# Kernel optimization log

Measured on AMD Instinct MI355X. Metric: run time of the kernel, lower is better.

## Reference

```python
import jax, jax.numpy as jnp
import numpy as np

N_NODES = 50000
N_GRAPHS = 512


def _gcn_layer(x, src, dst, W, b):
    # DGL GraphConv, norm='both', allow_zero_in_degree=True
    n = x.shape[0]
    ones = jnp.ones(src.shape[0], x.dtype)
    deg_out = jnp.zeros(n, x.dtype).at[src].add(ones)
    deg_in = jnp.zeros(n, x.dtype).at[dst].add(ones)
    norm_out = jax.lax.rsqrt(jnp.maximum(deg_out, 1.0))
    norm_in = jax.lax.rsqrt(jnp.maximum(deg_in, 1.0))
    h = x * norm_out[:, None]
    agg = jax.ops.segment_sum(h[src], dst, num_segments=n)  # SpMM
    return (agg * norm_in[:, None]) @ W + b


def setup_inputs() -> dict:
    key = jax.random.key(0)
    ks = jax.random.split(key, 16)
    E = 800000
    inp = {
        'nid': jax.random.randint(ks[0], (N_NODES,), 0, 100000),
        'z': jax.random.randint(ks[1], (N_NODES,), 0, 1000),
        'src': jax.random.randint(ks[2], (E,), 0, N_NODES),
        'dst': jax.random.randint(ks[3], (E,), 0, N_NODES),
        'graph_id': jnp.sort(jax.random.randint(ks[4], (N_NODES,), 0, N_GRAPHS)),
        'init_embed': jax.random.normal(ks[5], (100000, 64), jnp.float32) * 0.1,
        'z_table': jax.random.normal(ks[6], (1000, 64), jnp.float32) * 0.1,
        'W0': jax.random.normal(ks[7], (128, 128), jnp.float32) * 0.1,
        'b0': jnp.zeros((128,), jnp.float32),
        'W1': jax.random.normal(ks[8], (128, 128), jnp.float32) * 0.1,
        'b1': jnp.zeros((128,), jnp.float32),
        'W2': jax.random.normal(ks[9], (128, 128), jnp.float32) * 0.1,
        'b2': jnp.zeros((128,), jnp.float32),
        'lin1_W': jax.random.normal(ks[10], (128, 128), jnp.float32) * 0.1,
        'lin1_b': jnp.zeros((128,), jnp.float32),
        'lin2_W': jax.random.normal(ks[11], (128, 200), jnp.float32) * 0.1,
        'lin2_b': jnp.zeros((200,), jnp.float32),
    }
    return inp


def reference(nid, z, src, dst, graph_id, init_embed, z_table, W0, b0, W1, b1, W2, b2, lin1_W, lin1_b, lin2_W, lin2_b):
    # node features: entity embedding lookup + structural label embedding, concat
    x = jnp.concatenate([init_embed[nid], z_table[z]], axis=1)  # [N, 128]
    # layers[:-1] with relu (dropout is identity in eval mode)
    x = jax.nn.relu(_gcn_layer(x, src, dst, W0, b0))
    x = jax.nn.relu(_gcn_layer(x, src, dst, W1, b1))
    x = _gcn_layer(x, src, dst, W2, b2)
    # SumPooling over subgraphs in the batch
    g = jax.ops.segment_sum(x, graph_id, num_segments=N_GRAPHS)  # [G, 128]
    h = jax.nn.relu(g @ lin1_W + lin1_b)
    return h @ lin2_W + lin2_b  # [G, num_rel]
```

## Files before the change

kernel.cpp:

```cpp
#include <hip/hip_runtime.h>
#include <hip/hip_bf16.h>


#define FEAT 128
#define NG 512
#define CH 128
#define NPMAX 12544
#define LDW 136

typedef __attribute__((ext_vector_type(8))) short bf16x8;
typedef __attribute__((ext_vector_type(4))) float f32x4;

__device__ __forceinline__ float bf2f(unsigned short u) {
    union { unsigned int i; float f; } v; v.i = ((unsigned int)u) << 16; return v.f;
}
__device__ __forceinline__ unsigned short f2bf(float f) {
    unsigned int u = __float_as_uint(f);
    return (unsigned short)((u + 0x7FFFu + ((u >> 16) & 1u)) >> 16);
}
__device__ __forceinline__ float lo16(unsigned u) { return __uint_as_float(u << 16); }
__device__ __forceinline__ float hi16(unsigned u) { return __uint_as_float(u & 0xFFFF0000u); }

__global__ __launch_bounds__(256) void k_hist(
        const int* __restrict__ src, const int* __restrict__ dst,
        unsigned* __restrict__ partial_out, unsigned* __restrict__ partial_in,
        int E, int NP, int Ec) {
    __shared__ unsigned h[NPMAX];
    int tid = threadIdx.x;
    int b = blockIdx.x;
    int c = b & (CH - 1);
    const int* __restrict__ arr = (b < CH) ? src : dst;
    unsigned* __restrict__ outp = ((b < CH) ? partial_out : partial_in) + (size_t)c * NP;
    for (int i = tid; i < NP; i += 256) h[i] = 0;
    __syncthreads();
    int e0 = c * Ec, e1 = min(E, e0 + Ec);
    for (int e = e0 + tid; e < e1; e += 256) {
        int v = arr[e];
        atomicAdd(&h[v >> 2], 1u << ((v & 3) * 8));
    }
    __syncthreads();
    for (int i = tid; i < NP; i += 256) outp[i] = h[i];
}

__global__ void k_merge(unsigned* __restrict__ partial_out, unsigned* __restrict__ partial_in,
                        int* __restrict__ cnt_in, float* __restrict__ norm_out,
                        float* __restrict__ norm_in, int N, int NP) {
    int w = blockIdx.x * blockDim.x + threadIdx.x;
    if (w >= NP) return;
    unsigned run_in = 0, run_out = 0;
    for (int c = 0; c < CH; c++) {
        size_t idx = (size_t)c * NP + w;
        unsigned v = partial_in[idx];
        partial_in[idx] = run_in;
        run_in += v;
        run_out += partial_out[idx];
    }
    #pragma unroll
    for (int j = 0; j < 4; j++) {
        int node = w * 4 + j;
        if (node < N) {
            unsigned di = (run_in  >> (j * 8)) & 255u;
            unsigned dd = (run_out >> (j * 8)) & 255u;
            cnt_in[node]   = (int)di;
            norm_in[node]  = rsqrtf(fmaxf((float)di, 1.0f));
            norm_out[node] = rsqrtf(fmaxf((float)dd, 1.0f));
        }
    }
}

__global__ void k_scan_local(const int* __restrict__ cnt, int* __restrict__ excl,
                             int* __restrict__ bsum, int N) {
    __shared__ int s[256];
    int x = threadIdx.x;
    int i = blockIdx.x * 256 + x;
    int v = (i < N) ? cnt[i] : 0;
    s[x] = v;
    __syncthreads();
    for (int off = 1; off < 256; off <<= 1) {
        int t = (x >= off) ? s[x - off] : 0;
        __syncthreads();
        s[x] += t;
        __syncthreads();
    }
    if (i < N) excl[i] = s[x] - v;
    if (x == 255) bsum[blockIdx.x] = s[255];
}

__global__ void k_scan_bsum_prep(int* __restrict__ bsum, int* __restrict__ boff, int nb,
                                 const float* __restrict__ W0, const float* __restrict__ W1,
                                 unsigned short* __restrict__ WF0, unsigned short* __restrict__ WF1) {
    if (blockIdx.x == 0) {
        __shared__ int s[256];
        int x = threadIdx.x;
        int v = (x < nb) ? bsum[x] : 0;
        s[x] = v;
        __syncthreads();
        for (int off = 1; off < 256; off <<= 1) {
            int t = (x >= off) ? s[x - off] : 0;
            __syncthreads();
            s[x] += t;
            __syncthreads();
        }
        if (x < nb) boff[x] = s[x] - v;
    } else {
        int t = ((int)blockIdx.x - 1) * 256 + threadIdx.x;
        const float* __restrict__ W = (t < 16384) ? W0 : W1;
        unsigned short* __restrict__ WF = (t < 16384) ? WF0 : WF1;
        int tt = t & 16383;
        int f = tt >> 9, l = (tt >> 3) & 63, e = tt & 7;
        int n = (f >> 2) * 16 + (l & 15);
        int k = (f & 3) * 32 + (l >> 4) * 8 + e;
        WF[tt] = f2bf(W[k * 128 + n]);
    }
}

__global__ void k_add_off(int* __restrict__ row_start, const int* __restrict__ boff,
                          float* __restrict__ g, int N) {
    int i = blockIdx.x * blockDim.x + threadIdx.x;
    int stride = gridDim.x * blockDim.x;
    if (i < N) row_start[i] += boff[i >> 8];
    for (int j = i; j < NG * FEAT; j += stride) g[j] = 0.f;
}

__global__ __launch_bounds__(256) void k_fill_bx(
        const int* __restrict__ src, const int* __restrict__ dst,
        const int* __restrict__ row_start, const unsigned* __restrict__ partial_in,
        unsigned short* __restrict__ csr,
        const int* __restrict__ nid, const int* __restrict__ z,
        const float* __restrict__ emb, const float* __restrict__ zt,
        const float* __restrict__ nout, unsigned short* __restrict__ x,
        int N, int E, int NP, int Ec) {
    if ((int)blockIdx.x < CH) {
        __shared__ unsigned cur[NPMAX];
        int tid = threadIdx.x;
        int c = blockIdx.x;
        const unsigned* __restrict__ pre = partial_in + (size_t)c * NP;
        for (int i = tid; i < NP; i += 256) cur[i] = pre[i];
        __syncthreads();
        int e0 = c * Ec, e1 = min(E, e0 + Ec);
        for (int e = e0 + tid; e < e1; e += 256) {
            int d = dst[e], s = src[e];
            int sh = (d & 3) * 8;
            unsigned t = atomicAdd(&cur[d >> 2], 1u << sh);
            int off = (int)((t >> sh) & 255u);
            csr[row_start[d] + off] = (unsigned short)s;
        }
    } else {
        int tid = ((int)blockIdx.x - CH) * 256 + threadIdx.x;
        int i = tid >> 5, q = tid & 31;
        if (i < N) {
            float4 v;
            if (q < 16) v = ((const float4*)emb)[(size_t)nid[i] * 16 + q];
            else        v = ((const float4*)zt)[(size_t)z[i] * 16 + (q - 16)];
            float w = nout[i];
            ushort4 u;
            u.x = f2bf(v.x * w); u.y = f2bf(v.y * w);
            u.z = f2bf(v.z * w); u.w = f2bf(v.w * w);
            ((ushort4*)x)[(size_t)i * 32 + q] = u;
        }
    }
}

#define ACC8(u)                                                                  \
    a0 += lo16(u.x); a1 += hi16(u.x); a2 += lo16(u.y); a3 += hi16(u.y);          \
    a4 += lo16(u.z); a5 += hi16(u.z); a6 += lo16(u.w); a7 += hi16(u.w);

#define GATHER_LOOP                                                              \
    {                                                                            \
        int base = row_start[node];                                              \
        int n = cnt_in[node];                                                    \
        const uint4* xp = (const uint4*)x;                   \
        for (int j0 = 0; j0 < n; j0 += 16) {                                     \
            int rem = n - j0;                                                    \
            int m = rem < 16 ? rem : 16;                                         \
            int e = (int)csr[base + j0 + (ql < m ? ql : 0)];                     \
            int j = 0;                                                           \
            for (; j + 8 <= m; j += 8) {                                         \
                int s0 = __shfl(e, j + 0, 16), s1 = __shfl(e, j + 1, 16);        \
                int s2 = __shfl(e, j + 2, 16), s3 = __shfl(e, j + 3, 16);        \
                int s4 = __shfl(e, j + 4, 16), s5 = __shfl(e, j + 5, 16);        \
                int s6 = __shfl(e, j + 6, 16), s7 = __shfl(e, j + 7, 16);        \
                uint4 u0 = xp[(size_t)s0 * 16 + ql];                             \
                uint4 u1 = xp[(size_t)s1 * 16 + ql];                             \
                uint4 u2 = xp[(size_t)s2 * 16 + ql];                             \
                uint4 u3 = xp[(size_t)s3 * 16 + ql];                             \
                uint4 u4 = xp[(size_t)s4 * 16 + ql];                             \
                uint4 u5 = xp[(size_t)s5 * 16 + ql];                             \
                uint4 u6 = xp[(size_t)s6 * 16 + ql];                             \
                uint4 u7 = xp[(size_t)s7 * 16 + ql];                             \
                ACC8(u0) ACC8(u1) ACC8(u2) ACC8(u3)                              \
                ACC8(u4) ACC8(u5) ACC8(u6) ACC8(u7)                              \
            }                                                                    \
            for (; j + 4 <= m; j += 4) {                                         \
                int s0 = __shfl(e, j + 0, 16), s1 = __shfl(e, j + 1, 16);        \
                int s2 = __shfl(e, j + 2, 16), s3 = __shfl(e, j + 3, 16);        \
                uint4 u0 = xp[(size_t)s0 * 16 + ql];                             \
                uint4 u1 = xp[(size_t)s1 * 16 + ql];                             \
                uint4 u2 = xp[(size_t)s2 * 16 + ql];                             \
                uint4 u3 = xp[(size_t)s3 * 16 + ql];                             \
                ACC8(u0) ACC8(u1) ACC8(u2) ACC8(u3)                              \
            }                                                                    \
            for (; j < m; j++) {                                                 \
                int s = __shfl(e, j, 16);                                        \
                uint4 u = xp[(size_t)s * 16 + ql];                               \
                ACC8(u)                                                          \
            }                                                                    \
        }                                                                        \
    }

__global__ __launch_bounds__(256) void k_gather_gemm(
        const unsigned short* __restrict__ x, const float* __restrict__ nin,
        const unsigned short* __restrict__ csr, const int* __restrict__ row_start,
        const int* __restrict__ cnt_in, const unsigned short* __restrict__ WF,
        const float* __restrict__ bias, const float* __restrict__ nout,
        unsigned short* __restrict__ y, int N) {
    __shared__ unsigned short As[64 * LDW];
    int tid = threadIdx.x;
    int nb = blockIdx.x * 64;
    int ql = tid & 15;
    int nsub = tid >> 4;

    #pragma unroll 1
    for (int r = 0; r < 4; r++) {
        int node = nb + r * 16 + nsub;
        float a0 = 0.f, a1 = 0.f, a2 = 0.f, a3 = 0.f;
        float a4 = 0.f, a5 = 0.f, a6 = 0.f, a7 = 0.f;
        if (node < N) {
            GATHER_LOOP
            float ni = nin[node];
            a0 *= ni; a1 *= ni; a2 *= ni; a3 *= ni;
            a4 *= ni; a5 *= ni; a6 *= ni; a7 *= ni;
        }
        uint4 o;
        o.x = (unsigned)f2bf(a0) | ((unsigned)f2bf(a1) << 16);
        o.y = (unsigned)f2bf(a2) | ((unsigned)f2bf(a3) << 16);
        o.z = (unsigned)f2bf(a4) | ((unsigned)f2bf(a5) << 16);
        o.w = (unsigned)f2bf(a6) | ((unsigned)f2bf(a7) << 16);
        *(uint4*)(As + (r * 16 + nsub) * LDW + ql * 8) = o;
    }
    __syncthreads();

    int lane = tid & 63;
    int m0 = (tid >> 6) * 16;
    int c = lane & 15, q = lane >> 4;

    const unsigned short* ap = As + (m0 + c) * LDW + q * 8;
    bf16x8 fa0 = *(const bf16x8*)(ap);
    bf16x8 fa1 = *(const bf16x8*)(ap + 32);
    bf16x8 fa2 = *(const bf16x8*)(ap + 64);
    bf16x8 fa3 = *(const bf16x8*)(ap + 96);
    const bf16x8* __restrict__ wf = (const bf16x8*)WF;

    #pragma unroll
    for (int nt = 0; nt < 8; nt++) {
        bf16x8 fb0 = wf[(nt * 4 + 0) * 64 + lane];
        bf16x8 fb1 = wf[(nt * 4 + 1) * 64 + lane];
        bf16x8 fb2 = wf[(nt * 4 + 2) * 64 + lane];
        bf16x8 fb3 = wf[(nt * 4 + 3) * 64 + lane];
        float bb = bias[nt * 16 + c];
        f32x4 acc = {bb, bb, bb, bb};
        acc = __builtin_amdgcn_mfma_f32_16x16x32_bf16(fa0, fb0, acc, 0, 0, 0);
        acc = __builtin_amdgcn_mfma_f32_16x16x32_bf16(fa1, fb1, acc, 0, 0, 0);
        acc = __builtin_amdgcn_mfma_f32_16x16x32_bf16(fa2, fb2, acc, 0, 0, 0);
        acc = __builtin_amdgcn_mfma_f32_16x16x32_bf16(fa3, fb3, acc, 0, 0, 0);
        #pragma unroll
        for (int rr = 0; rr < 4; rr++) {
            int row = m0 + q * 4 + rr;
            float s = nout[min(nb + row, N - 1)];
            As[row * LDW + nt * 16 + c] = f2bf(fmaxf(acc[rr], 0.f) * s);
        }
    }
    __syncthreads();

    for (int i = tid; i < 64 * 16; i += 256) {
        int row = i >> 4, seg = i & 15;
        int node = nb + row;
        if (node < N) {
            const ushort4* p = (const ushort4*)(As + row * LDW + seg * 8);
            ushort4* d = (ushort4*)(y + (size_t)node * 128 + seg * 8);
            d[0] = p[0]; d[1] = p[1];
        }
    }
}

__global__ __launch_bounds__(256) void k_gather_pool(
        const unsigned short* __restrict__ x, const float* __restrict__ nin,
        const unsigned short* __restrict__ csr, const int* __restrict__ row_start,
        const int* __restrict__ cnt_in, const int* __restrict__ gid,
        float* __restrict__ g, int N) {
    __shared__ float gl[16][FEAT];
    __shared__ int used;
    int tid = threadIdx.x;
    int nb = blockIdx.x * 16;
    for (int i = tid; i < 16 * FEAT; i += 256) ((float*)gl)[i] = 0.f;
    if (tid == 0) used = 0;
    __syncthreads();

    int ql = tid & 15;
    int node = nb + (tid >> 4);
    int g0 = gid[nb];
    float a0 = 0.f, a1 = 0.f, a2 = 0.f, a3 = 0.f;
    float a4 = 0.f, a5 = 0.f, a6 = 0.f, a7 = 0.f;
    int slot = -1;
    if (node < N) {
        GATHER_LOOP
        float ni = nin[node];
        a0 *= ni; a1 *= ni; a2 *= ni; a3 *= ni;
        a4 *= ni; a5 *= ni; a6 *= ni; a7 *= ni;
        slot = gid[node] - g0;
    }
    if (slot >= 16) {
        float* p = g + (size_t)(g0 + slot) * FEAT + ql * 8;
        atomicAdd(p + 0, a0); atomicAdd(p + 1, a1);
        atomicAdd(p + 2, a2); atomicAdd(p + 3, a3);
        atomicAdd(p + 4, a4); atomicAdd(p + 5, a5);
        atomicAdd(p + 6, a6); atomicAdd(p + 7, a7);
    } else if (slot >= 0) {
        float* p = &gl[slot][ql * 8];
        atomicAdd(p + 0, a0); atomicAdd(p + 1, a1);
        atomicAdd(p + 2, a2); atomicAdd(p + 3, a3);
        atomicAdd(p + 4, a4); atomicAdd(p + 5, a5);
        atomicAdd(p + 6, a6); atomicAdd(p + 7, a7);
        if (ql == 0) atomicOr(&used, 1 << slot);
    }
    __syncthreads();
    int u = used;
    #pragma unroll
    for (int s0 = 0; s0 < 16; s0 += 2) {
        int s = s0 + (tid >> 7);
        if ((u >> s) & 1) {
            int j = tid & 127;
            atomicAdd(&g[(size_t)(g0 + s) * FEAT + j], gl[s][j]);
        }
    }
}

__global__ __launch_bounds__(256) void k_head(
        const float* __restrict__ g, const int* __restrict__ gid,
        const float* __restrict__ W2, const float* __restrict__ b2,
        const float* __restrict__ l1W, const float* __restrict__ l1b,
        const float* __restrict__ l2W, const float* __restrict__ l2b,
        float* __restrict__ out, int N) {
    __shared__ float gs[128];
    __shared__ float ys[128];
    __shared__ float hs[128];
    int gi = blockIdx.x, tid = threadIdx.x;

    int lo = 0, hi = N;
    while (lo < hi) { int m = (lo + hi) >> 1; if (gid[m] < gi) lo = m + 1; else hi = m; }
    int s0 = lo;
    lo = 0; hi = N;
    while (lo < hi) { int m = (lo + hi) >> 1; if (gid[m] < gi + 1) lo = m + 1; else hi = m; }
    float cnt = (float)(lo - s0);

    if (tid < 128) gs[tid] = g[(size_t)gi * FEAT + tid];
    __syncthreads();
    if (tid < 128) {
        float a = cnt * b2[tid];
        for (int k = 0; k < 128; k++) a += gs[k] * W2[(size_t)k * 128 + tid];
        ys[tid] = a;
    }
    __syncthreads();
    if (tid < 128) {
        float a = l1b[tid];
        for (int k = 0; k < 128; k++) a += ys[k] * l1W[(size_t)k * 128 + tid];
        hs[tid] = fmaxf(a, 0.f);
    }
    __syncthreads();
    if (tid < 200) {
        float a = l2b[tid];
        for (int k = 0; k < 128; k++) a += hs[k] * l2W[(size_t)k * 200 + tid];
        out[(size_t)gi * 200 + tid] = a;
    }
}

extern "C" void kernel_launch(void* const* d_in, const int* in_sizes, int n_in,
                              void* d_out, int out_size, void* d_ws, size_t ws_size,
                              hipStream_t stream) {
    const int*   nid = (const int*)d_in[0];
    const int*   z   = (const int*)d_in[1];
    const int*   src = (const int*)d_in[2];
    const int*   dst = (const int*)d_in[3];
    const int*   gid = (const int*)d_in[4];
    const float* emb = (const float*)d_in[5];
    const float* zt  = (const float*)d_in[6];
    const float* W0  = (const float*)d_in[7];
    const float* b0  = (const float*)d_in[8];
    const float* W1  = (const float*)d_in[9];
    const float* b1  = (const float*)d_in[10];
    const float* W2  = (const float*)d_in[11];
    const float* b2  = (const float*)d_in[12];
    const float* l1W = (const float*)d_in[13];
    const float* l1b = (const float*)d_in[14];
    const float* l2W = (const float*)d_in[15];
    const float* l2b = (const float*)d_in[16];
    float* out = (float*)d_out;

    const int N = in_sizes[0];
    const int E = in_sizes[2];
    const int NB = (N + 255) / 256;
    const int NP = (N + 3) / 4;
    const int Ec = (E + CH - 1) / CH;

    size_t NA = (size_t)((N + 63) & ~63);
    float* norm_out = (float*)d_ws;
    float* norm_in  = norm_out + NA;
    float* g        = norm_in + NA;
    unsigned short* xA  = (unsigned short*)(g + (size_t)NG * FEAT);
    unsigned short* xB  = xA + (size_t)N * FEAT;
    unsigned short* WF0 = xB + (size_t)N * FEAT;
    unsigned short* WF1 = WF0 + 128 * 128;
    int* cnt_in    = (int*)(WF1 + 128 * 128);
    int* row_start = cnt_in + NA;
    int* bsum      = row_start + NA;
    int* boff      = bsum + 256;
    unsigned* partial_out = (unsigned*)(boff + 256);
    unsigned* partial_in  = partial_out + (size_t)CH * NP;
    unsigned short* csr = (unsigned short*)(partial_in + (size_t)CH * NP);

    k_hist<<<2 * CH, 256, 0, stream>>>(src, dst, partial_out, partial_in, E, NP, Ec);
    k_merge<<<(NP + 255) / 256, 256, 0, stream>>>(partial_out, partial_in, cnt_in,
                                                  norm_out, norm_in, N, NP);
    k_scan_local<<<NB, 256, 0, stream>>>(cnt_in, row_start, bsum, N);
    k_scan_bsum_prep<<<1 + 128, 256, 0, stream>>>(bsum, boff, NB, W0, W1, WF0, WF1);
    k_add_off<<<NB, 256, 0, stream>>>(row_start, boff, g, N);
    int XB = (N * 32 + 255) / 256;
    k_fill_bx<<<CH + XB, 256, 0, stream>>>(src, dst, row_start, partial_in, csr,
                                           nid, z, emb, zt, norm_out, xA, N, E, NP, Ec);

    int gg_blocks = (N + 63) / 64;
    int gp_blocks = (N + 15) / 16;

    k_gather_gemm<<<gg_blocks, 256, 0, stream>>>(xA, norm_in, csr, row_start, cnt_in,
                                                 WF0, b0, norm_out, xB, N);
    k_gather_gemm<<<gg_blocks, 256, 0, stream>>>(xB, norm_in, csr, row_start, cnt_in,
                                                 WF1, b1, norm_out, xA, N);
    k_gather_pool<<<gp_blocks, 256, 0, stream>>>(xA, norm_in, csr, row_start, cnt_in,
                                                 gid, g, N);

    k_head<<<NG, 256, 0, stream>>>(g, gid, W2, b2, l1W, l1b, l2W, l2b, out, N);
}
```

Before: 313.0 us.

## Shrink gather-GEMM tiles to 16 nodes and segment-reduce pooling in shared memory

The gather-GEMM kernel now handles 16 nodes per block instead of 64. Each of the four waves computes two of the eight 16-column output tiles over the same 16 rows, so there are four times as many blocks and no serial four-pass gather loop. This should raise parallelism and latency hiding in the memory-bound gather, at the cost of reloading the weight fragments per block. The pooling kernel replaces per-element LDS atomics and the used-mask with a plain store to shared memory, then a run-length segmented sum over sorted graph ids, issuing one global atomic per run.

Result: faster. 277.8 us (-11.2%).

```diff
diff --git a/kernel.cpp b/kernel.cpp
--- a/kernel.cpp
+++ b/kernel.cpp
@@ -214,45 +214,44 @@
         const int* __restrict__ cnt_in, const unsigned short* __restrict__ WF,
         const float* __restrict__ bias, const float* __restrict__ nout,
         unsigned short* __restrict__ y, int N) {
-    __shared__ unsigned short As[64 * LDW];
+    __shared__ unsigned short As[16 * LDW];
     int tid = threadIdx.x;
-    int nb = blockIdx.x * 64;
+    int nb = blockIdx.x * 16;
     int ql = tid & 15;
-    int nsub = tid >> 4;
-
-    #pragma unroll 1
-    for (int r = 0; r < 4; r++) {
-        int node = nb + r * 16 + nsub;
-        float a0 = 0.f, a1 = 0.f, a2 = 0.f, a3 = 0.f;
-        float a4 = 0.f, a5 = 0.f, a6 = 0.f, a7 = 0.f;
-        if (node < N) {
-            GATHER_LOOP
-            float ni = nin[node];
-            a0 *= ni; a1 *= ni; a2 *= ni; a3 *= ni;
-            a4 *= ni; a5 *= ni; a6 *= ni; a7 *= ni;
-        }
-        uint4 o;
-        o.x = (unsigned)f2bf(a0) | ((unsigned)f2bf(a1) << 16);
-        o.y = (unsigned)f2bf(a2) | ((unsigned)f2bf(a3) << 16);
-        o.z = (unsigned)f2bf(a4) | ((unsigned)f2bf(a5) << 16);
-        o.w = (unsigned)f2bf(a6) | ((unsigned)f2bf(a7) << 16);
-        *(uint4*)(As + (r * 16 + nsub) * LDW + ql * 8) = o;
-    }
+    int nl = tid >> 4;
+    int node = nb + nl;
+
+    float a0 = 0.f, a1 = 0.f, a2 = 0.f, a3 = 0.f;
+    float a4 = 0.f, a5 = 0.f, a6 = 0.f, a7 = 0.f;
+    if (node < N) {
+        GATHER_LOOP
+        float ni = nin[node];
+        a0 *= ni; a1 *= ni; a2 *= ni; a3 *= ni;
+        a4 *= ni; a5 *= ni; a6 *= ni; a7 *= ni;
+    }
+    uint4 o;
+    o.x = (unsigned)f2bf(a0) | ((unsigned)f2bf(a1) << 16);
+    o.y = (unsigned)f2bf(a2) | ((unsigned)f2bf(a3) << 16);
+    o.z = (unsigned)f2bf(a4) | ((unsigned)f2bf(a5) << 16);
+    o.w = (unsigned)f2bf(a6) | ((unsigned)f2bf(a7) << 16);
+    *(uint4*)(As + nl * LDW + ql * 8) = o;
     __syncthreads();
 
     int lane = tid & 63;
-    int m0 = (tid >> 6) * 16;
+    int wv = tid >> 6;
     int c = lane & 15, q = lane >> 4;
 
-    const unsigned short* ap = As + (m0 + c) * LDW + q * 8;
+    const unsigned short* ap = As + c * LDW + q * 8;
     bf16x8 fa0 = *(const bf16x8*)(ap);
     bf16x8 fa1 = *(const bf16x8*)(ap + 32);
     bf16x8 fa2 = *(const bf16x8*)(ap + 64);
     bf16x8 fa3 = *(const bf16x8*)(ap + 96);
     const bf16x8* __restrict__ wf = (const bf16x8*)WF;
+    __syncthreads();
 
     #pragma unroll
-    for (int nt = 0; nt < 8; nt++) {
+    for (int t = 0; t < 2; t++) {
+        int nt = wv * 2 + t;
         bf16x8 fb0 = wf[(nt * 4 + 0) * 64 + lane];
         bf16x8 fb1 = wf[(nt * 4 + 1) * 64 + lane];
         bf16x8 fb2 = wf[(nt * 4 + 2) * 64 + lane];
@@ -265,19 +264,19 @@
         acc = __builtin_amdgcn_mfma_f32_16x16x32_bf16(fa3, fb3, acc, 0, 0, 0);
         #pragma unroll
         for (int rr = 0; rr < 4; rr++) {
-            int row = m0 + q * 4 + rr;
+            int row = q * 4 + rr;
             float s = nout[min(nb + row, N - 1)];
             As[row * LDW + nt * 16 + c] = f2bf(fmaxf(acc[rr], 0.f) * s);
         }
     }
     __syncthreads();
 
-    for (int i = tid; i < 64 * 16; i += 256) {
-        int row = i >> 4, seg = i & 15;
-        int node = nb + row;
-        if (node < N) {
+    {
+        int row = tid >> 4, seg = tid & 15;
+        int nd = nb + row;
+        if (nd < N) {
             const ushort4* p = (const ushort4*)(As + row * LDW + seg * 8);
-            ushort4* d = (ushort4*)(y + (size_t)node * 128 + seg * 8);
+            ushort4* d = (ushort4*)(y + (size_t)nd * 128 + seg * 8);
             d[0] = p[0]; d[1] = p[1];
         }
     }
@@ -288,17 +287,14 @@
         const unsigned short* __restrict__ csr, const int* __restrict__ row_start,
         const int* __restrict__ cnt_in, const int* __restrict__ gid,
         float* __restrict__ g, int N) {
-    __shared__ float gl[16][FEAT];
-    __shared__ int used;
+    __shared__ __align__(16) float gl[16][132];
+    __shared__ int slots[16];
     int tid = threadIdx.x;
     int nb = blockIdx.x * 16;
-    for (int i = tid; i < 16 * FEAT; i += 256) ((float*)gl)[i] = 0.f;
-    if (tid == 0) used = 0;
-    __syncthreads();
-
     int ql = tid & 15;
-    int node = nb + (tid >> 4);
-    int g0 = gid[nb];
+    int nl = tid >> 4;
+    int node = nb + nl;
+
     float a0 = 0.f, a1 = 0.f, a2 = 0.f, a3 = 0.f;
     float a4 = 0.f, a5 = 0.f, a6 = 0.f, a7 = 0.f;
     int slot = -1;
@@ -307,32 +303,29 @@
         float ni = nin[node];
         a0 *= ni; a1 *= ni; a2 *= ni; a3 *= ni;
         a4 *= ni; a5 *= ni; a6 *= ni; a7 *= ni;
-        slot = gid[node] - g0;
-    }
-    if (slot >= 16) {
-        float* p = g + (size_t)(g0 + slot) * FEAT + ql * 8;
-        atomicAdd(p + 0, a0); atomicAdd(p + 1, a1);
-        atomicAdd(p + 2, a2); atomicAdd(p + 3, a3);
-        atomicAdd(p + 4, a4); atomicAdd(p + 5, a5);
-        atomicAdd(p + 6, a6); atomicAdd(p + 7, a7);
-    } else if (slot >= 0) {
-        float* p = &gl[slot][ql * 8];
-        atomicAdd(p + 0, a0); atomicAdd(p + 1, a1);
-        atomicAdd(p + 2, a2); atomicAdd(p + 3, a3);
-        atomicAdd(p + 4, a4); atomicAdd(p + 5, a5);
-        atomicAdd(p + 6, a6); atomicAdd(p + 7, a7);
-        if (ql == 0) atomicOr(&used, 1 << slot);
-    }
-    __syncthreads();
-    int u = used;
+        slot = gid[node];
+    }
+    float4* row = (float4*)&gl[nl][ql * 8];
+    row[0] = make_float4(a0, a1, a2, a3);
+    row[1] = make_float4(a4, a5, a6, a7);
+    if (ql == 0) slots[nl] = slot;
+    __syncthreads();
+
+    int h = tid >> 7;
+    int j = tid & 127;
+    int prev = -1;
+    float acc = 0.f;
     #pragma unroll
-    for (int s0 = 0; s0 < 16; s0 += 2) {
-        int s = s0 + (tid >> 7);
-        if ((u >> s) & 1) {
-            int j = tid & 127;
-            atomicAdd(&g[(size_t)(g0 + s) * FEAT + j], gl[s][j]);
-        }
-    }
+    for (int i = h * 8; i < h * 8 + 8; i++) {
+        int s = slots[i];
+        if (s != prev) {
+            if (prev >= 0) atomicAdd(&g[(size_t)prev * FEAT + j], acc);
+            acc = 0.f;
+            prev = s;
+        }
+        acc += gl[i][j];
+    }
+    if (prev >= 0) atomicAdd(&g[(size_t)prev * FEAT + j], acc);
 }
 
 __global__ __launch_bounds__(256) void k_head(
@@ -428,14 +421,13 @@
     k_fill_bx<<<CH + XB, 256, 0, stream>>>(src, dst, row_start, partial_in, csr,
                                            nid, z, emb, zt, norm_out, xA, N, E, NP, Ec);
 
-    int gg_blocks = (N + 63) / 64;
-    int gp_blocks = (N + 15) / 16;
+    int gg_blocks = (N + 15) / 16;
 
     k_gather_gemm<<<gg_blocks, 256, 0, stream>>>(xA, norm_in, csr, row_start, cnt_in,
                                                  WF0, b0, norm_out, xB, N);
     k_gather_gemm<<<gg_blocks, 256, 0, stream>>>(xB, norm_in, csr, row_start, cnt_in,
                                                  WF1, b1, norm_out, xA, N);
-    k_gather_pool<<<gp_blocks, 256, 0, stream>>>(xA, norm_in, csr, row_start, cnt_in,
+    k_gather_pool<<<gg_blocks, 256, 0, stream>>>(xA, norm_in, csr, row_start, cnt_in,
                                                  gid, g, N);
 
     k_head<<<NG, 256, 0, stream>>>(g, gid, W2, b2, l1W, l1b, l2W, l2b, out, N);
```
